# Kernel tuning notes

Measured on AMD Instinct MI355X. Metric: run time of the kernel, lower is better.

Reference implementation:

```python
import jax, jax.numpy as jnp
import numpy as np

N = 50000      # nodes
E = 800000     # edges (before self-loops)
G = 64         # graphs
F_IN = 128     # n_attr
OUT = 128      # size_vect
NEG_SLOPE = 0.2


def setup_inputs() -> dict:
    key = jax.random.key(0)
    ks = jax.random.split(key, 48)
    def rn(i, shape, s=0.05):
        return (jax.random.normal(ks[i], shape, jnp.float32) * s)
    x = jax.random.normal(ks[0], (N, F_IN), jnp.float32)
    src = jax.random.randint(ks[1], (E,), 0, N, jnp.int32)
    dst = jax.random.randint(ks[2], (E,), 0, N, jnp.int32)
    dst = jnp.where(dst == src, (dst + 1) % N, dst)  # no pre-existing self-loops
    edge_index = jnp.stack([src, dst])
    batch = jnp.sort(jax.random.randint(ks[3], (N,), 0, G, jnp.int32))
    inp = {"x": x, "edge_index": edge_index, "batch": batch}
    # GATConv params (heads=1): W [in,out], att_src/att_dst [out], bias [out]
    dims = [(F_IN, 64), (64, 128), (128, 256)]
    for li, (di, do) in enumerate(dims, start=1):
        b = 4 + (li - 1) * 4
        inp[f"W{li}"] = rn(b, (di, do))
        inp[f"asrc{li}"] = rn(b + 1, (do,))
        inp[f"adst{li}"] = rn(b + 2, (do,))
        inp[f"b{li}"] = rn(b + 3, (do,))
    # dense tail: Linear stored as [in,out]
    dense = {"d1": (512, 256), "d2": (256, 128), "d3": (128, 64),
             "mean": (256, 64), "d4": (64, 64), "d5": (64, 128),
             "d6": (128, 256), "d7": (256, OUT)}
    i = 20
    for name, (di, do) in dense.items():
        inp[f"{name}_w"] = rn(i, (di, do))
        inp[f"{name}_b"] = rn(i + 1, (do,))
        i += 2
    return inp


def _gat_conv(x, src, dst, W, a_src, a_dst, b):
    h = x @ W                                   # [N, out]
    e = (h @ a_src)[src] + (h @ a_dst)[dst]     # [E']
    e = jnp.where(e > 0, e, NEG_SLOPE * e)      # LeakyReLU(0.2)
    m = jax.ops.segment_max(e, dst, num_segments=N)
    ex = jnp.exp(e - m[dst])
    denom = jax.ops.segment_sum(ex, dst, num_segments=N)
    alpha = ex / denom[dst]                     # segment softmax over incoming edges
    out = jax.ops.segment_sum(h[src] * alpha[:, None], dst, num_segments=N)
    return out + b


def reference(x, edge_index, batch,
              W1, asrc1, adst1, b1, W2, asrc2, adst2, b2, W3, asrc3, adst3, b3,
              d1_w, d1_b, d2_w, d2_b, d3_w, d3_b, mean_w, mean_b,
              d4_w, d4_b, d5_w, d5_b, d6_w, d6_b, d7_w, d7_b):
    ar = jnp.arange(N, dtype=edge_index.dtype)
    src = jnp.concatenate([edge_index[0], ar])  # add self-loops (PyG default)
    dst = jnp.concatenate([edge_index[1], ar])
    h = _gat_conv(x, src, dst, W1, asrc1, adst1, b1)
    h = _gat_conv(h, src, dst, W2, asrc2, adst2, b2)
    h = _gat_conv(h, src, dst, W3, asrc3, adst3, b3)   # [N, 256]
    x1 = jax.ops.segment_max(h, batch, num_segments=G)
    x2 = jax.ops.segment_sum(h, batch, num_segments=G)
    cnt = jax.ops.segment_sum(jnp.ones((N,), h.dtype), batch, num_segments=G)
    x3 = x2 / jnp.maximum(cnt, 1.0)[:, None]
    z = jnp.concatenate([x1, x2], axis=-1)              # [G, 512]
    z = jax.nn.relu(z @ d1_w + d1_b)
    z = jax.nn.relu(z @ d2_w + d2_b)
    z = jax.nn.relu(z @ d3_w + d3_b)
    z = z * jax.nn.sigmoid(x3 @ mean_w + mean_b)
    z = jax.nn.relu(z @ d4_w + d4_b)                    # dropout = identity (eval)
    z = jax.nn.relu(z @ d5_w + d5_b)
    z = jax.nn.relu(z @ d6_w + d6_b)
    return z @ d7_w + d7_b
```

## Files before the change

### kernel.cpp

```cpp
#include <hip/hip_runtime.h>
#include <hip/hip_bf16.h>
#include <math.h>

#define NN 50000
#define NE 800000
#define NEP 850000
#define NG 64
#define CAP 64

#define NBKT 49
#define BMAX 20480
#define EPB  3125
#define KE   13

typedef unsigned short u16;
typedef __attribute__((ext_vector_type(8))) short short8;
typedef __attribute__((ext_vector_type(4))) float f32x4;

__device__ __forceinline__ float bfu2f(u16 u) {
    return __uint_as_float((unsigned)u << 16);
}
__device__ __forceinline__ u16 f2bfu(float f) {
    __hip_bfloat16 h = __float2bfloat16(f);
    union { __hip_bfloat16 h; u16 u; } c; c.h = h; return c.u;
}

__device__ __forceinline__ unsigned fkey(float f) {
    unsigned u = __float_as_uint(f);
    return (u & 0x80000000u) ? ~u : (u | 0x80000000u);
}
__device__ __forceinline__ float fkey_inv(unsigned k) {
    return (k & 0x80000000u) ? __uint_as_float(k ^ 0x80000000u) : __uint_as_float(~k);
}

__global__ void k_init(int* __restrict__ deg, u16* __restrict__ srcsort,
                       int* __restrict__ poolbuf, int IB,
                       const float* __restrict__ W0, const float* __restrict__ as0, const float* __restrict__ ad0,
                       u16* __restrict__ Wb0, float* __restrict__ wa0, float* __restrict__ wb0,
                       const float* __restrict__ W1, const float* __restrict__ as1, const float* __restrict__ ad1,
                       u16* __restrict__ Wb1, float* __restrict__ wa1, float* __restrict__ wb1,
                       const float* __restrict__ W2, const float* __restrict__ as2, const float* __restrict__ ad2,
                       const float* __restrict__ b2f, const float* __restrict__ b3f,
                       u16* __restrict__ Wcb, float* __restrict__ bcv,
                       float* __restrict__ wa2c, float* __restrict__ wb2c,
                       float* __restrict__ cst) {
    __shared__ float pas[4], pbs[4];
    int tid = threadIdx.x;
    if (blockIdx.x < IB) {
        int i = blockIdx.x * 256 + tid;
        if (i < NN) {
            deg[i] = 1;
            srcsort[i << 6] = (u16)i;
        } else if (i - NN < NG * 512 + NG + 64) {
            poolbuf[i - NN] = 0;
        }
        return;
    }
    int b = blockIdx.x - IB;
    if (b < 192) {
        const float *W, *asv, *adv; u16* Wb; float *wa, *wb; int k, dout;
        if (b < 128) { W = W0; asv = as0; adv = ad0; Wb = Wb0; wa = wa0; wb = wb0; k = b;       dout = 64;  }
        else         { W = W1; asv = as1; adv = ad1; Wb = Wb1; wa = wa1; wb = wb1; k = b - 128; dout = 128; }
        float pa = 0.f, pb = 0.f;
        for (int n = tid; n < dout; n += 256) {
            float w = W[(size_t)k * dout + n];
            Wb[(size_t)k * dout + n] = f2bfu(w);
            pa += w * asv[n];
            pb += w * adv[n];
        }
#pragma unroll
        for (int off = 32; off; off >>= 1) {
            pa += __shfl_xor(pa, off);
            pb += __shfl_xor(pb, off);
        }
        if ((tid & 63) == 0) { pas[tid >> 6] = pa; pbs[tid >> 6] = pb; }
        __syncthreads();
        if (tid == 0) {
            wa[k] = pas[0] + pas[1] + pas[2] + pas[3];
            wb[k] = pbs[0] + pbs[1] + pbs[2] + pbs[3];
        }
        return;
    }
    if (b < 256) {
        int k = b - 192;
        int o = tid;
        float wc = 0.f;
        const float* wrow = W1 + (size_t)k * 128;
#pragma unroll 4
        for (int j = 0; j < 128; j++) wc += wrow[j] * W2[(size_t)j * 256 + o];
        Wcb[(size_t)k * 256 + o] = f2bfu(wc);
        float pa = wc * as2[o];
        float pb = wc * ad2[o];
#pragma unroll
        for (int off = 32; off; off >>= 1) {
            pa += __shfl_xor(pa, off);
            pb += __shfl_xor(pb, off);
        }
        if ((tid & 63) == 0) { pas[tid >> 6] = pa; pbs[tid >> 6] = pb; }
        __syncthreads();
        if (tid == 0) {
            wa2c[k] = pas[0] + pas[1] + pas[2] + pas[3];
            wb2c[k] = pbs[0] + pbs[1] + pbs[2] + pbs[3];
        }
        return;
    }
    {
        int o = tid;
        float t = 0.f;
#pragma unroll 4
        for (int j = 0; j < 128; j++) t += b2f[j] * W2[(size_t)j * 256 + o];
        bcv[o] = t + b3f[o];
        float ps = t * as2[o];
        float pt = t * ad2[o];
#pragma unroll
        for (int off = 32; off; off >>= 1) {
            ps += __shfl_xor(ps, off);
            pt += __shfl_xor(pt, off);
        }
        if ((tid & 63) == 0) { pas[tid >> 6] = ps; pbs[tid >> 6] = pt; }
        __syncthreads();
        if (tid == 0) {
            cst[0] = pas[0] + pas[1] + pas[2] + pas[3];
            cst[1] = pbs[0] + pbs[1] + pbs[2] + pbs[3];
        }
    }
}

__global__ __launch_bounds__(256) void k_bin(const int* __restrict__ src, const int* __restrict__ dst,
                                             unsigned* __restrict__ ebuf, int* __restrict__ bcur) {
    __shared__ int hist[NBKT], gbase[NBKT];
    int tid = threadIdx.x;
    int e0 = blockIdx.x * EPB;
    if (tid < NBKT) hist[tid] = 0;
    __syncthreads();
    unsigned pk[KE];
    unsigned br[KE];
#pragma unroll
    for (int k = 0; k < KE; k++) {
        int e = tid + k * 256;
        pk[k] = 0; br[k] = 0xffffffffu;
        if (e < EPB) {
            int sv = src[e0 + e];
            int dv = dst[e0 + e];
            int bkt = dv >> 10;
            int r = atomicAdd(&hist[bkt], 1);
            pk[k] = (unsigned)sv | ((unsigned)(dv & 1023) << 16);
            br[k] = ((unsigned)bkt << 16) | (unsigned)r;
        }
    }
    __syncthreads();
    if (tid < NBKT) gbase[tid] = atomicAdd(&bcur[tid], hist[tid]);
    __syncthreads();
#pragma unroll
    for (int k = 0; k < KE; k++) {
        if (br[k] != 0xffffffffu) {
            int bkt = (int)(br[k] >> 16);
            int r   = (int)(br[k] & 0xffffu);
            ebuf[(size_t)bkt * BMAX + gbase[bkt] + r] = pk[k];
        }
    }
}

template<int DIN, int DOUT, bool XF32, bool STIN>
__device__ __forceinline__ void gemm_body(int bx, const void* __restrict__ Xin,
                                          const u16* __restrict__ Wb,
                                          u16* __restrict__ Hb,
                                          const float* __restrict__ bias,
                                          const float* __restrict__ wav,
                                          const float* __restrict__ wbv,
                                          float* __restrict__ sout,
                                          float* __restrict__ tout) {
    constexpr int KS = DIN / 32;
    constexpr int CT = DOUT / 16;
    constexpr int TPW = CT / 4;
    constexpr int STRIDE = DIN + 16;
    __shared__ u16 Xs[64 * STRIDE];
    int tid = threadIdx.x, wave = tid >> 6, lane = tid & 63;
    int quad = lane >> 4, l15 = lane & 15;
    int n0 = bx * 64;

    short8 bfr[TPW][KS];
#pragma unroll
    for (int ct = 0; ct < TPW; ct++) {
        int nb = (wave * TPW + ct) * 16 + l15;
#pragma unroll
        for (int ks = 0; ks < KS; ks++) {
            int kb = ks * 32 + quad * 8;
            short8 b;
#pragma unroll
            for (int j = 0; j < 8; j++) b[j] = (short)Wb[(size_t)(kb + j) * DOUT + nb];
            bfr[ct][ks] = b;
        }
    }

    for (int c = tid; c < 64 * DIN / 8; c += 256) {
        int row = (c * 8) / DIN, col = (c * 8) % DIN;
        int rg = n0 + row; if (rg >= NN) rg = NN - 1;
        u16 v[8];
        if constexpr (XF32) {
            const float* p = (const float*)Xin + (size_t)rg * DIN + col;
            float4 f0 = *(const float4*)p;
            float4 f1 = *(const float4*)(p + 4);
            v[0] = f2bfu(f0.x); v[1] = f2bfu(f0.y); v[2] = f2bfu(f0.z); v[3] = f2bfu(f0.w);
            v[4] = f2bfu(f1.x); v[5] = f2bfu(f1.y); v[6] = f2bfu(f1.z); v[7] = f2bfu(f1.w);
            if constexpr (STIN) {
                float pa = f0.x * wav[col]     + f0.y * wav[col + 1]
                         + f0.z * wav[col + 2] + f0.w * wav[col + 3]
                         + f1.x * wav[col + 4] + f1.y * wav[col + 5]
                         + f1.z * wav[col + 6] + f1.w * wav[col + 7];
                float pb = f0.x * wbv[col]     + f0.y * wbv[col + 1]
                         + f0.z * wbv[col + 2] + f0.w * wbv[col + 3]
                         + f1.x * wbv[col + 4] + f1.y * wbv[col + 5]
                         + f1.z * wbv[col + 6] + f1.w * wbv[col + 7];
                constexpr int RT = DIN / 8;
#pragma unroll
                for (int off = RT / 2; off; off >>= 1) {
                    pa += __shfl_xor(pa, off);
                    pb += __shfl_xor(pb, off);
                }
                if ((tid & (RT - 1)) == 0 && (n0 + row) < NN) {
                    sout[n0 + row] = pa;
                    tout[n0 + row] = pb;
                }
            }
        } else {
            const u16* p = (const u16*)Xin + (size_t)rg * DIN + col;
            ushort4 a = *(const ushort4*)p;
            ushort4 b = *(const ushort4*)(p + 4);
            v[0] = a.x; v[1] = a.y; v[2] = a.z; v[3] = a.w;
            v[4] = b.x; v[5] = b.y; v[6] = b.z; v[7] = b.w;
        }
        u16* d = &Xs[row * STRIDE + col];
#pragma unroll
        for (int j = 0; j < 8; j++) d[j] = v[j];
    }
    __syncthreads();

#pragma unroll
    for (int rt = 0; rt < 4; rt++) {
        short8 afr[KS];
#pragma unroll
        for (int ks = 0; ks < KS; ks++)
            afr[ks] = *(const short8*)&Xs[(rt * 16 + l15) * STRIDE + ks * 32 + quad * 8];
#pragma unroll
        for (int ct = 0; ct < TPW; ct++) {
            f32x4 cf = {0.f, 0.f, 0.f, 0.f};
#pragma unroll
            for (int ks = 0; ks < KS; ks++)
                cf = __builtin_amdgcn_mfma_f32_16x16x32_bf16(afr[ks], bfr[ct][ks], cf, 0, 0, 0);
            int col = (wave * TPW + ct) * 16 + l15;
            float bv = bias ? bias[col] : 0.f;
            int rbase = n0 + rt * 16 + quad * 4;
#pragma unroll
            for (int reg = 0; reg < 4; reg++) {
                int r = rbase + reg;
                if (r < NN) Hb[(size_t)r * DOUT + col] = f2bfu(cf[reg] + bv);
            }
        }
    }
}

__global__ __launch_bounds__(256) void k_front(const unsigned* __restrict__ ebuf,
                                               const int* __restrict__ bcur,
                                               int* __restrict__ deg, u16* __restrict__ srcsort,
                                               const float* __restrict__ x_in,
                                               const u16* __restrict__ Wb0, u16* __restrict__ Hb,
                                               const float* __restrict__ wa, const float* __restrict__ wb,
                                               float* __restrict__ s, float* __restrict__ t) {
    int tid = threadIdx.x;
    if (blockIdx.x < NBKT) {
        __shared__ int cnt[1024];
        int bkt = blockIdx.x;
        int base = bkt << 10;
        for (int i = tid; i < 1024; i += 256) cnt[i] = 1;
        __syncthreads();
        int n = bcur[bkt];
        const unsigned* eb = ebuf + (size_t)bkt * BMAX;
        for (int e = tid; e < n; e += 256) {
            unsigned p = eb[e];
            int sv = (int)(p & 0xffffu);
            int dl = (int)(p >> 16);
            int pos = atomicAdd(&cnt[dl], 1);
            if (pos < CAP) srcsort[((base + dl) << 6) + pos] = (u16)sv;
        }
        __syncthreads();
        for (int i = tid; i < 1024; i += 256) {
            int node = base + i;
            if (node < NN) deg[node] = cnt[i];
        }
        return;
    }
    gemm_body<128, 64, true, true>(blockIdx.x - NBKT, x_in, Wb0, Hb, nullptr, wa, wb, s, t);
}

template<int DIN, int DOUT>
__global__ __launch_bounds__(256) void k_gemm_b(const u16* __restrict__ Xin,
                                                const u16* __restrict__ Wb,
                                                u16* __restrict__ Hb,
                                                const float* __restrict__ bias) {
    gemm_body<DIN, DOUT, false, false>(blockIdx.x, Xin, Wb, Hb, bias,
                                       nullptr, nullptr, nullptr, nullptr);
}

template<bool BIAS>
__global__ void k_agg1(const int* __restrict__ deg, const u16* __restrict__ srcsort,
                       const float* __restrict__ s, const float* __restrict__ t,
                       const u16* __restrict__ Hb, const float* __restrict__ bias,
                       u16* __restrict__ OUT, const float* __restrict__ wan,
                       const float* __restrict__ wbn, const float* __restrict__ cst,
                       float* __restrict__ sout, float* __restrict__ tout) {
    constexpr int GS = 8;
    constexpr int P  = 8;
    int node = blockIdx.x * 4 + (threadIdx.x >> 6);
    int lane = threadIdx.x & 63;
    if (node >= NN) return;
    int cnt = min(deg[node], CAP);
    float tn = t[node];
    int sv = 0; float ex = 0.f;
    if (lane < cnt) {
        sv = srcsort[(node << 6) + lane];
        float e = s[sv] + tn;
        e = (e > 0.f) ? e : 0.2f * e;
        ex = expf(e);
    }
    float dsum = ex;
#pragma unroll
    for (int off = 32; off; off >>= 1) dsum += __shfl_xor(dsum, off);
    ex *= 1.f / dsum;

    int sg = lane / GS;
    int pg = lane % GS;
    float acc[8];
#pragma unroll
    for (int e = 0; e < 8; e++) acc[e] = 0.f;

    for (int q = 0; q < cnt; q += P) {
        int myq = q + sg;
        int mq = (myq < cnt) ? myq : q;
        float a = __shfl(ex, mq);
        int  idx = __shfl(sv, mq);
        if (myq >= cnt) a = 0.f;
        uint4 u = *(const uint4*)(Hb + (size_t)idx * 64 + pg * 8);
        acc[0] += a * bfu2f((u16)(u.x & 0xffff));
        acc[1] += a * bfu2f((u16)(u.x >> 16));
        acc[2] += a * bfu2f((u16)(u.y & 0xffff));
        acc[3] += a * bfu2f((u16)(u.y >> 16));
        acc[4] += a * bfu2f((u16)(u.z & 0xffff));
        acc[5] += a * bfu2f((u16)(u.z >> 16));
        acc[6] += a * bfu2f((u16)(u.w & 0xffff));
        acc[7] += a * bfu2f((u16)(u.w >> 16));
    }

#pragma unroll
    for (int step = GS; step < 64; step <<= 1) {
#pragma unroll
        for (int e = 0; e < 8; e++) acc[e] += __shfl_xor(acc[e], step);
    }
    if constexpr (BIAS) {
#pragma unroll
        for (int e = 0; e < 8; e++) acc[e] += bias[pg * 8 + e];
    }

    {
        float pa = 0.f, pb = 0.f;
#pragma unroll
        for (int e = 0; e < 8; e++) {
            pa += acc[e] * wan[pg * 8 + e];
            pb += acc[e] * wbn[pg * 8 + e];
        }
#pragma unroll
        for (int off = 32; off; off >>= 1) {
            pa += __shfl_xor(pa, off);
            pb += __shfl_xor(pb, off);
        }
        if (lane == 0) {
            float cs = 0.f, ct_ = 0.f;
            if constexpr (!BIAS) { cs = cst[0]; ct_ = cst[1]; }
            sout[node] = pa * (1.f / P) + cs;
            tout[node] = pb * (1.f / P) + ct_;
        }
    }

    if (sg == 0) {
        uint4 o;
        o.x = (unsigned)f2bfu(acc[0]) | ((unsigned)f2bfu(acc[1]) << 16);
        o.y = (unsigned)f2bfu(acc[2]) | ((unsigned)f2bfu(acc[3]) << 16);
        o.z = (unsigned)f2bfu(acc[4]) | ((unsigned)f2bfu(acc[5]) << 16);
        o.w = (unsigned)f2bfu(acc[6]) | ((unsigned)f2bfu(acc[7]) << 16);
        *(uint4*)(OUT + (size_t)node * 64 + pg * 8) = o;
    }
}

template<int DIN>
__global__ void k_aggX(const int* __restrict__ deg, const u16* __restrict__ srcsort,
                       const float* __restrict__ s, const float* __restrict__ t,
                       const u16* __restrict__ X, u16* __restrict__ OUT) {
    constexpr int GS = DIN / 8;
    constexpr int P  = 64 / GS;
    int node = blockIdx.x * 4 + (threadIdx.x >> 6);
    int lane = threadIdx.x & 63;
    if (node >= NN) return;
    int cnt = min(deg[node], CAP);
    float tn = t[node];
    int sv = 0; float ex = 0.f;
    if (lane < cnt) {
        sv = srcsort[(node << 6) + lane];
        float e = s[sv] + tn;
        e = (e > 0.f) ? e : 0.2f * e;
        ex = expf(e);
    }
    float dsum = ex;
#pragma unroll
    for (int off = 32; off; off >>= 1) dsum += __shfl_xor(dsum, off);
    ex *= 1.f / dsum;

    int sg = lane / GS;
    int pg = lane % GS;
    float acc[8];
#pragma unroll
    for (int e = 0; e < 8; e++) acc[e] = 0.f;

    for (int q = 0; q < cnt; q += P) {
        int myq = q + sg;
        int mq = (myq < cnt) ? myq : q;
        float a = __shfl(ex, mq);
        int  idx = __shfl(sv, mq);
        if (myq >= cnt) a = 0.f;
        uint4 u = *(const uint4*)(X + (size_t)idx * DIN + pg * 8);
        acc[0] += a * bfu2f((u16)(u.x & 0xffff));
        acc[1] += a * bfu2f((u16)(u.x >> 16));
        acc[2] += a * bfu2f((u16)(u.y & 0xffff));
        acc[3] += a * bfu2f((u16)(u.y >> 16));
        acc[4] += a * bfu2f((u16)(u.z & 0xffff));
        acc[5] += a * bfu2f((u16)(u.z >> 16));
        acc[6] += a * bfu2f((u16)(u.w & 0xffff));
        acc[7] += a * bfu2f((u16)(u.w >> 16));
    }

#pragma unroll
    for (int step = GS; step < 64; step <<= 1) {
#pragma unroll
        for (int e = 0; e < 8; e++) acc[e] += __shfl_xor(acc[e], step);
    }

    if (sg == 0) {
        uint4 o;
        o.x = (unsigned)f2bfu(acc[0]) | ((unsigned)f2bfu(acc[1]) << 16);
        o.y = (unsigned)f2bfu(acc[2]) | ((unsigned)f2bfu(acc[3]) << 16);
        o.z = (unsigned)f2bfu(acc[4]) | ((unsigned)f2bfu(acc[5]) << 16);
        o.w = (unsigned)f2bfu(acc[6]) | ((unsigned)f2bfu(acc[7]) << 16);
        *(uint4*)(OUT + (size_t)node * DIN + pg * 8) = o;
    }
}

__global__ void k_pool2(const u16* __restrict__ H, const int* __restrict__ batch,
                        unsigned* __restrict__ x1k, float* __restrict__ x2,
                        float* __restrict__ cnt) {
    int c0 = blockIdx.x * 64;
    if (c0 >= NN) return;
    int o = threadIdx.x;
    int endn = min(c0 + 64, NN);
    int g = batch[c0];
    float mx = -INFINITY, sm = 0.f, cl = 0.f;
    for (int nd = c0; nd < endn; nd++) {
        int bg = batch[nd];
        if (bg != g) {
            atomicMax(&x1k[g * 256 + o], fkey(mx));
            atomicAdd(&x2[g * 256 + o], sm);
            if (o == 0) atomicAdd(&cnt[g], cl);
            g = bg; mx = -INFINITY; sm = 0.f; cl = 0.f;
        }
        float hv = bfu2f(H[(size_t)nd * 256 + o]);
        mx = fmaxf(mx, hv);
        sm += hv;
        cl += 1.f;
    }
    atomicMax(&x1k[g * 256 + o], fkey(mx));
    atomicAdd(&x2[g * 256 + o], sm);
    if (o == 0) atomicAdd(&cnt[g], cl);
}

template<int DIN, int DOUT, int ACT>
__device__ __forceinline__ void dense_layer(const float* __restrict__ in,
                                            const float* __restrict__ W,
                                            const float* __restrict__ B,
                                            float* __restrict__ out, int o,
                                            float* __restrict__ red) {
    constexpr int T = 1024 / DOUT;
    constexpr int KS = DIN / T;
    int oo = o % DOUT;
    int kk = o / DOUT;
    int kbase = kk * KS;
    float p0 = 0.f, p1 = 0.f, p2 = 0.f, p3 = 0.f;
#pragma unroll 4
    for (int k = 0; k < KS; k += 4) {
        p0 += in[kbase + k]     * W[(size_t)(kbase + k) * DOUT + oo];
        p1 += in[kbase + k + 1] * W[(size_t)(kbase + k + 1) * DOUT + oo];
        p2 += in[kbase + k + 2] * W[(size_t)(kbase + k + 2) * DOUT + oo];
        p3 += in[kbase + k + 3] * W[(size_t)(kbase + k + 3) * DOUT + oo];
    }
    float p = (p0 + p1) + (p2 + p3);
    red[o] = p;
    __syncthreads();
    if (o < DOUT) {
#pragma unroll
        for (int tt = 1; tt < T; tt++) p += red[oo + tt * DOUT];
        p += B[oo];
        if constexpr (ACT == 1) p = fmaxf(p, 0.f);
        else if constexpr (ACT == 2) p = 1.f / (1.f + expf(-p));
        out[oo] = p;
    }
    __syncthreads();
}

__global__ __launch_bounds__(1024) void k_tail(const unsigned* __restrict__ x1k, const float* __restrict__ x2,
                       const float* __restrict__ cnt,
                       const float* __restrict__ d1w, const float* __restrict__ d1b,
                       const float* __restrict__ d2w, const float* __restrict__ d2b,
                       const float* __restrict__ d3w, const float* __restrict__ d3b,
                       const float* __restrict__ mw,  const float* __restrict__ mb,
                       const float* __restrict__ d4w, const float* __restrict__ d4b,
                       const float* __restrict__ d5w, const float* __restrict__ d5b,
                       const float* __restrict__ d6w, const float* __restrict__ d6b,
                       const float* __restrict__ d7w, const float* __restrict__ d7b,
                       float* __restrict__ out) {
    __shared__ float z[512];
    __shared__ float A[256];
    __shared__ float Bf[256];
    __shared__ float red[1024];
    __shared__ float x3s[256];
    __shared__ float gbuf[64];
    int g = blockIdx.x, o = threadIdx.x;
    if (o < 256) {
        float c = fmaxf(cnt[g], 1.f);
        float sv = x2[(size_t)g * 256 + o];
        z[o] = fkey_inv(x1k[(size_t)g * 256 + o]);
        z[256 + o] = sv;
        x3s[o] = sv / c;
    }
    __syncthreads();
    dense_layer<512, 256, 1>(z,   d1w, d1b, A,    o, red);
    dense_layer<256, 128, 1>(A,   d2w, d2b, Bf,   o, red);
    dense_layer<128,  64, 1>(Bf,  d3w, d3b, A,    o, red);
    dense_layer<256,  64, 2>(x3s, mw,  mb,  gbuf, o, red);
    if (o < 64) A[o] *= gbuf[o];
    __syncthreads();
    dense_layer< 64,  64, 1>(A,   d4w, d4b, Bf,   o, red);
    dense_layer< 64, 128, 1>(Bf,  d5w, d5b, A,    o, red);
    dense_layer<128, 256, 1>(A,   d6w, d6b, z,    o, red);
    dense_layer<256, 128, 0>(z,   d7w, d7b, A,    o, red);
    if (o < 128) out[(size_t)g * 128 + o] = A[o];
}

extern "C" void kernel_launch(void* const* d_in, const int* in_sizes, int n_in,
                              void* d_out, int out_size, void* d_ws, size_t ws_size,
                              hipStream_t stream) {
    const float* x_in  = (const float*)d_in[0];
    const int*   ei    = (const int*)d_in[1];
    const int*   batch = (const int*)d_in[2];
    const int* src = ei;
    const int* dst = ei + NE;

    const float* Wl[3]  = { (const float*)d_in[3], (const float*)d_in[7],  (const float*)d_in[11] };
    const float* asl[3] = { (const float*)d_in[4], (const float*)d_in[8],  (const float*)d_in[12] };
    const float* adl[3] = { (const float*)d_in[5], (const float*)d_in[9],  (const float*)d_in[13] };
    const float* bl[3]  = { (const float*)d_in[6], (const float*)d_in[10], (const float*)d_in[14] };

    const float* d1w = (const float*)d_in[15]; const float* d1b = (const float*)d_in[16];
    const float* d2w = (const float*)d_in[17]; const float* d2b = (const float*)d_in[18];
    const float* d3w = (const float*)d_in[19]; const float* d3b = (const float*)d_in[20];
    const float* mw  = (const float*)d_in[21]; const float* mb  = (const float*)d_in[22];
    const float* d4w = (const float*)d_in[23]; const float* d4b = (const float*)d_in[24];
    const float* d5w = (const float*)d_in[25]; const float* d5b = (const float*)d_in[26];
    const float* d6w = (const float*)d_in[27]; const float* d6b = (const float*)d_in[28];
    const float* d7w = (const float*)d_in[29]; const float* d7b = (const float*)d_in[30];

    float* ws = (float*)d_ws;
    size_t off = 0;
    u16* Hb1 = (u16*)(ws + off); off += (size_t)NN * 32;
    u16* Xb1 = (u16*)(ws + off); off += (size_t)NN * 32;
    u16* A2  = (u16*)(ws + off); off += (size_t)NN * 32;
    u16* B3  = (u16*)(ws + off); off += (size_t)NN * 64;
    float* bcv = ws + off; off += 256;
    float* cst = ws + off; off += 64;
    u16* Xb3 = (u16*)(ws + off); off += (size_t)NN * 128;
    float* sA = ws + off; off += NN;
    float* tA = ws + off; off += NN;
    float* sB = ws + off; off += NN;
    float* tB = ws + off; off += NN;
    u16* Wb0 = (u16*)(ws + off); off += (128 * 64) / 2;
    u16* Wb1 = (u16*)(ws + off); off += (64 * 128) / 2;
    u16* Wcb = (u16*)(ws + off); off += (64 * 256) / 2;
    float* wa0 = ws + off; off += 128;  float* wb0 = ws + off; off += 128;
    float* wa1 = ws + off; off += 64;   float* wb1 = ws + off; off += 64;
    float* wa2c = ws + off; off += 64;  float* wb2c = ws + off; off += 64;
    unsigned* x1k = (unsigned*)(ws + off); off += NG * 256;
    float* x2    = ws + off; off += NG * 256;
    float* cnt   = ws + off; off += NG;
    int* bcur    = (int*)(ws + off); off += 64;
    int* ip      = (int*)(ws + off);
    int* deg     = ip;               ip += NN;
    u16* srcsort = (u16*)ip;         ip += (NN * CAP) / 2;
    unsigned* ebuf = (unsigned*)Xb3;

    const int GB = (NN + 63) / 64;
    const int AB = (NN + 3) / 4;
    const int IB = (NN + NG * 512 + NG + 64 + 255) / 256;

    k_init<<<IB + 257, 256, 0, stream>>>(deg, srcsort, (int*)x1k, IB,
                                         Wl[0], asl[0], adl[0], Wb0, wa0, wb0,
                                         Wl[1], asl[1], adl[1], Wb1, wa1, wb1,
                                         Wl[2], asl[2], adl[2], bl[1], bl[2],
                                         Wcb, bcv, wa2c, wb2c, cst);
    k_bin<<<256, 256, 0, stream>>>(src, dst, ebuf, bcur);
    k_front<<<NBKT + GB, 256, 0, stream>>>(ebuf, bcur, deg, srcsort,
                                           x_in, Wb0, Hb1, wa0, wb0, sA, tA);

    k_agg1<true><<<AB, 256, 0, stream>>>(deg, srcsort, sA, tA, Hb1, bl[0],
                                         Xb1, wa1, wb1, nullptr, sB, tB);

    k_agg1<false><<<AB, 256, 0, stream>>>(deg, srcsort, sB, tB, Xb1, nullptr,
                                          A2, wa2c, wb2c, cst, sA, tA);

    k_aggX<64><<<AB, 256, 0, stream>>>(deg, srcsort, sA, tA, A2, B3);
    k_gemm_b<64, 256><<<GB, 256, 0, stream>>>(B3, Wcb, Xb3, bcv);

    k_pool2<<<(NN + 63) / 64, 256, 0, stream>>>(Xb3, batch, x1k, x2, cnt);
    k_tail<<<NG, 1024, 0, stream>>>(x1k, x2, cnt,
                                    d1w, d1b, d2w, d2b, d3w, d3b, mw, mb,
                                    d4w, d4b, d5w, d5b, d6w, d6b, d7w, d7b,
                                    (float*)d_out);
}
```

Baseline: 321.2 us.

## Fuse final GAT projection GEMM with graph max/sum pooling

The last projection GEMM now keeps its MFMA accumulators in registers and reduces them straight into per-graph max and sum with shuffles and atomics. This replaces writing the [N,256] bf16 layer output and reading it back in a separate pooling kernel, and saves one launch. The price is more accumulator registers (possible occupancy loss), a loop over the graphs present in each 64-row tile, and a serial per-block count loop on one thread. The edge bucket buffer gets its own workspace slot, since it can no longer alias the removed output buffer.

```diff
diff --git a/kernel.cpp b/kernel.cpp
--- a/kernel.cpp
+++ b/kernel.cpp
@@ -161,7 +161,7 @@
     }
 }
 
-template<int DIN, int DOUT, bool XF32, bool STIN>
+template<int DIN, int DOUT, bool XF32, bool STIN, bool POOL>
 __device__ __forceinline__ void gemm_body(int bx, const void* __restrict__ Xin,
                                           const u16* __restrict__ Wb,
                                           u16* __restrict__ Hb,
@@ -169,12 +169,17 @@
                                           const float* __restrict__ wav,
                                           const float* __restrict__ wbv,
                                           float* __restrict__ sout,
-                                          float* __restrict__ tout) {
+                                          float* __restrict__ tout,
+                                          const int* __restrict__ batch,
+                                          unsigned* __restrict__ x1k,
+                                          float* __restrict__ x2,
+                                          float* __restrict__ cnt) {
     constexpr int KS = DIN / 32;
     constexpr int CT = DOUT / 16;
     constexpr int TPW = CT / 4;
     constexpr int STRIDE = DIN + 16;
     __shared__ u16 Xs[64 * STRIDE];
+    __shared__ int gID[64];
     int tid = threadIdx.x, wave = tid >> 6, lane = tid & 63;
     int quad = lane >> 4, l15 = lane & 15;
     int n0 = bx * 64;
@@ -190,6 +195,13 @@
 #pragma unroll
             for (int j = 0; j < 8; j++) b[j] = (short)Wb[(size_t)(kb + j) * DOUT + nb];
             bfr[ct][ks] = b;
+        }
+    }
+
+    if constexpr (POOL) {
+        if (tid < 64) {
+            int rg = n0 + tid;
+            gID[tid] = batch[(rg < NN) ? rg : (NN - 1)];
         }
     }
 
@@ -236,6 +248,7 @@
     }
     __syncthreads();
 
+    f32x4 acc[4][TPW];
 #pragma unroll
     for (int rt = 0; rt < 4; rt++) {
         short8 afr[KS];
@@ -248,14 +261,71 @@
 #pragma unroll
             for (int ks = 0; ks < KS; ks++)
                 cf = __builtin_amdgcn_mfma_f32_16x16x32_bf16(afr[ks], bfr[ct][ks], cf, 0, 0, 0);
-            int col = (wave * TPW + ct) * 16 + l15;
-            float bv = bias ? bias[col] : 0.f;
-            int rbase = n0 + rt * 16 + quad * 4;
-#pragma unroll
-            for (int reg = 0; reg < 4; reg++) {
-                int r = rbase + reg;
-                if (r < NN) Hb[(size_t)r * DOUT + col] = f2bfu(cf[reg] + bv);
+            if constexpr (POOL) {
+                acc[rt][ct] = cf;
+            } else {
+                int col = (wave * TPW + ct) * 16 + l15;
+                float bv = bias ? bias[col] : 0.f;
+                int rbase = n0 + rt * 16 + quad * 4;
+#pragma unroll
+                for (int reg = 0; reg < 4; reg++) {
+                    int r = rbase + reg;
+                    if (r < NN) Hb[(size_t)r * DOUT + col] = f2bfu(cf[reg] + bv);
+                }
             }
+        }
+    }
+
+    if constexpr (POOL) {
+        float bv[TPW];
+#pragma unroll
+        for (int ct = 0; ct < TPW; ct++) bv[ct] = bias[(wave * TPW + ct) * 16 + l15];
+        int gmin = gID[0];
+        int lastv = (n0 + 63 < NN) ? 63 : (NN - 1 - n0);
+        int gmax = gID[lastv];
+        for (int g = gmin; g <= gmax; g++) {
+            float m[TPW], ss[TPW];
+#pragma unroll
+            for (int ct = 0; ct < TPW; ct++) { m[ct] = -INFINITY; ss[ct] = 0.f; }
+#pragma unroll
+            for (int rt = 0; rt < 4; rt++) {
+#pragma unroll
+                for (int reg = 0; reg < 4; reg++) {
+                    int lr = rt * 16 + quad * 4 + reg;
+                    bool ok = (n0 + lr < NN) && (gID[lr] == g);
+#pragma unroll
+                    for (int ct = 0; ct < TPW; ct++) {
+                        float v = acc[rt][ct][reg] + bv[ct];
+                        if (ok) { m[ct] = fmaxf(m[ct], v); ss[ct] += v; }
+                    }
+                }
+            }
+#pragma unroll
+            for (int ct = 0; ct < TPW; ct++) {
+                m[ct]  = fmaxf(m[ct],  __shfl_xor(m[ct], 16));
+                ss[ct] += __shfl_xor(ss[ct], 16);
+                m[ct]  = fmaxf(m[ct],  __shfl_xor(m[ct], 32));
+                ss[ct] += __shfl_xor(ss[ct], 32);
+            }
+            if (lane < 16) {
+#pragma unroll
+                for (int ct = 0; ct < TPW; ct++) {
+                    int col = (wave * TPW + ct) * 16 + l15;
+                    if (m[ct] > -INFINITY) {
+                        atomicMax(&x1k[(size_t)g * 256 + col], fkey(m[ct]));
+                        atomicAdd(&x2[(size_t)g * 256 + col], ss[ct]);
+                    }
+                }
+            }
+        }
+        if (tid == 0) {
+            int cg = gID[0], cc = 0;
+            for (int i = 0; i < 64; i++) {
+                if (n0 + i >= NN) break;
+                if (gID[i] != cg) { atomicAdd(&cnt[cg], (float)cc); cg = gID[i]; cc = 0; }
+                cc++;
+            }
+            if (cc > 0) atomicAdd(&cnt[cg], (float)cc);
         }
     }
 }
@@ -290,16 +360,21 @@
         }
         return;
     }
-    gemm_body<128, 64, true, true>(blockIdx.x - NBKT, x_in, Wb0, Hb, nullptr, wa, wb, s, t);
+    gemm_body<128, 64, true, true, false>(blockIdx.x - NBKT, x_in, Wb0, Hb, nullptr, wa, wb, s, t,
+                                          nullptr, nullptr, nullptr, nullptr);
 }
 
 template<int DIN, int DOUT>
-__global__ __launch_bounds__(256) void k_gemm_b(const u16* __restrict__ Xin,
-                                                const u16* __restrict__ Wb,
-                                                u16* __restrict__ Hb,
-                                                const float* __restrict__ bias) {
-    gemm_body<DIN, DOUT, false, false>(blockIdx.x, Xin, Wb, Hb, bias,
-                                       nullptr, nullptr, nullptr, nullptr);
+__global__ __launch_bounds__(256) void k_gemm_pool(const u16* __restrict__ Xin,
+                                                   const u16* __restrict__ Wb,
+                                                   const float* __restrict__ bias,
+                                                   const int* __restrict__ batch,
+                                                   unsigned* __restrict__ x1k,
+                                                   float* __restrict__ x2,
+                                                   float* __restrict__ cnt) {
+    gemm_body<DIN, DOUT, false, false, true>(blockIdx.x, Xin, Wb, nullptr, bias,
+                                             nullptr, nullptr, nullptr, nullptr,
+                                             batch, x1k, x2, cnt);
 }
 
 template<bool BIAS>
@@ -451,33 +526,6 @@
         o.w = (unsigned)f2bfu(acc[6]) | ((unsigned)f2bfu(acc[7]) << 16);
         *(uint4*)(OUT + (size_t)node * DIN + pg * 8) = o;
     }
-}
-
-__global__ void k_pool2(const u16* __restrict__ H, const int* __restrict__ batch,
-                        unsigned* __restrict__ x1k, float* __restrict__ x2,
-                        float* __restrict__ cnt) {
-    int c0 = blockIdx.x * 64;
-    if (c0 >= NN) return;
-    int o = threadIdx.x;
-    int endn = min(c0 + 64, NN);
-    int g = batch[c0];
-    float mx = -INFINITY, sm = 0.f, cl = 0.f;
-    for (int nd = c0; nd < endn; nd++) {
-        int bg = batch[nd];
-        if (bg != g) {
-            atomicMax(&x1k[g * 256 + o], fkey(mx));
-            atomicAdd(&x2[g * 256 + o], sm);
-            if (o == 0) atomicAdd(&cnt[g], cl);
-            g = bg; mx = -INFINITY; sm = 0.f; cl = 0.f;
-        }
-        float hv = bfu2f(H[(size_t)nd * 256 + o]);
-        mx = fmaxf(mx, hv);
-        sm += hv;
-        cl += 1.f;
-    }
-    atomicMax(&x1k[g * 256 + o], fkey(mx));
-    atomicAdd(&x2[g * 256 + o], sm);
-    if (o == 0) atomicAdd(&cnt[g], cl);
 }
 
 template<int DIN, int DOUT, int ACT>
@@ -583,7 +631,7 @@
     u16* B3  = (u16*)(ws + off); off += (size_t)NN * 64;
     float* bcv = ws + off; off += 256;
     float* cst = ws + off; off += 64;
-    u16* Xb3 = (u16*)(ws + off); off += (size_t)NN * 128;
+    unsigned* ebuf = (unsigned*)(ws + off); off += (size_t)NBKT * BMAX;
     float* sA = ws + off; off += NN;
     float* tA = ws + off; off += NN;
     float* sB = ws + off; off += NN;
@@ -601,7 +649,6 @@
     int* ip      = (int*)(ws + off);
     int* deg     = ip;               ip += NN;
     u16* srcsort = (u16*)ip;         ip += (NN * CAP) / 2;
-    unsigned* ebuf = (unsigned*)Xb3;
 
     const int GB = (NN + 63) / 64;
     const int AB = (NN + 3) / 4;
@@ -623,9 +670,8 @@
                                           A2, wa2c, wb2c, cst, sA, tA);
 
     k_aggX<64><<<AB, 256, 0, stream>>>(deg, srcsort, sA, tA, A2, B3);
-    k_gemm_b<64, 256><<<GB, 256, 0, stream>>>(B3, Wcb, Xb3, bcv);
-
-    k_pool2<<<(NN + 63) / 64, 256, 0, stream>>>(Xb3, batch, x1k, x2, cnt);
+    k_gemm_pool<64, 256><<<GB, 256, 0, stream>>>(B3, Wcb, bcv, batch, x1k, x2, cnt);
+
     k_tail<<<NG, 1024, 0, stream>>>(x1k, x2, cnt,
                                     d1w, d1b, d2w, d2b, d3w, d3b, mw, mb,
                                     d4w, d4b, d5w, d5b, d6w, d6b, d7w, d7b,
```

New measurement: 302.3 us. 1.06x faster.
